# Performance work log

Hardware: AMD Instinct MI355X
Metric: run time of the kernel (lower is better)

The kernel has to match this reference:

```python
import jax, jax.numpy as jnp
import numpy as np

B, D = 16384, 2048          # batch, input_dim
N_TOP, N_CLASS = 8, 16      # top labels, bottom labels per top (uniform, contiguous ids)

def setup_inputs() -> dict:
    key = jax.random.key(0)
    k1, k2, k3, k4, k5 = jax.random.split(key, 5)
    INIT = 0.2  # matches init_weight uniform(-0.2, 0.2)
    return {
        "features": jax.random.normal(k1, (B, D), dtype=jnp.float32),
        "top_W": jax.random.uniform(k2, (N_TOP, D), minval=-INIT, maxval=INIT, dtype=jnp.float32),
        "top_b": jax.random.uniform(k3, (N_TOP,), minval=-INIT, maxval=INIT, dtype=jnp.float32),
        "bottom_W": jax.random.uniform(k4, (N_TOP, D, N_CLASS), minval=-INIT, maxval=INIT, dtype=jnp.float32),
        "bottom_b": jax.random.uniform(k5, (N_TOP, N_CLASS), minval=-INIT, maxval=INIT, dtype=jnp.float32),
    }

def reference(features, top_W, top_b, bottom_W, bottom_b):
    # dropout p=0.0 -> identity
    # top gate: linear + sigmoid, (b, n_top)
    top_scores = jax.nn.sigmoid(features @ top_W.T + top_b)
    # all per-top-label expert linears as one batched GEMM: (b, n_top, n_class)
    bottom_logits = jnp.einsum('bd,tdc->btc', features, bottom_W) + bottom_b
    bottom_scores = jax.nn.softmax(bottom_logits, axis=-1)
    # scatter-combine: bottom ids of top i are contiguous [i*N_CLASS, (i+1)*N_CLASS),
    # so the column scatter is a reshape. (b, n_bottom_labels)
    final_scores = (top_scores[:, :, None] * bottom_scores).reshape(features.shape[0], N_TOP * N_CLASS)
    return final_scores
```

## Files before the change

kernel.cpp:

```cpp
#include <hip/hip_runtime.h>


#define D_DIM 2048
#define NTILE 9
#define NCOLS 144

using f32x4 = float __attribute__((ext_vector_type(4)));
using half8 = _Float16 __attribute__((ext_vector_type(8)));

__global__ void prep_weights(const float* __restrict__ topW,
                             const float* __restrict__ botW,
                             _Float16* __restrict__ S) {
    int idx = blockIdx.x * blockDim.x + threadIdx.x;
    if (idx >= 4 * 16 * NTILE * 64) return;
    int lane = idx & 63;
    int tmp  = idx >> 6;
    int nt   = tmp % NTILE;
    int wks  = tmp / NTILE;
    int n     = nt * 16 + (lane & 15);
    int kbase = wks * 32 + (lane >> 4) * 8;

    _Float16 v[8];
    #pragma unroll
    for (int j = 0; j < 8; j++) {
        int k = kbase + j;
        float x = 0.0f;
        if (n < 8) {
            x = topW[n * D_DIM + k];
        } else if (n < 136) {
            int t = (n - 8) >> 4, c = (n - 8) & 15;
            x = botW[(t * D_DIM + k) * 16 + c];
        }
        v[j] = (_Float16)x;
    }
    *(half8*)(S + (size_t)idx * 8) = *(half8*)v;
}

__global__ __launch_bounds__(256, 4) void hc_fused(
        const float* __restrict__ feat, const _Float16* __restrict__ Bsw,
        const float* __restrict__ top_b, const float* __restrict__ bot_b,
        float* __restrict__ out) {
    __shared__ float red[4][16][148];

    const int tid  = threadIdx.x;
    const int lane = tid & 63, wave = tid >> 6;
    const int quad = lane >> 4, low = lane & 15;
    const size_t row0 = (size_t)blockIdx.x * 16;

    const f32x4* Ap = (const f32x4*)(feat + (row0 + low) * D_DIM + wave * 512 + quad * 8);
    const _Float16* Bw = Bsw + (size_t)wave * (16 * NTILE * 512) + lane * 8;

    f32x4 acc[NTILE];
    #pragma unroll
    for (int i = 0; i < NTILE; i++) acc[i] = (f32x4)0.0f;

    #pragma unroll 4
    for (int ks = 0; ks < 16; ks++) {
        f32x4 a0 = Ap[ks * 8];
        f32x4 a1 = Ap[ks * 8 + 1];
        half8 bf[NTILE];
        #pragma unroll
        for (int nt = 0; nt < NTILE; nt++)
            bf[nt] = *(const half8*)(Bw + (ks * NTILE + nt) * 512);
        half8 af;
        af[0] = (_Float16)a0[0]; af[1] = (_Float16)a0[1];
        af[2] = (_Float16)a0[2]; af[3] = (_Float16)a0[3];
        af[4] = (_Float16)a1[0]; af[5] = (_Float16)a1[1];
        af[6] = (_Float16)a1[2]; af[7] = (_Float16)a1[3];
        #pragma unroll
        for (int nt = 0; nt < NTILE; nt++)
            acc[nt] = __builtin_amdgcn_mfma_f32_16x16x32_f16(af, bf[nt], acc[nt], 0, 0, 0);
    }

    #pragma unroll
    for (int nt = 0; nt < NTILE; nt++) {
        #pragma unroll
        for (int r = 0; r < 4; r++) {
            red[wave][quad * 4 + r][nt * 16 + low] = acc[nt][r];
        }
    }
    __syncthreads();

    const int row = tid >> 4;
    const int top = tid & 15;
    if (top < 8) {
        float zt = top_b[top];
        #pragma unroll
        for (int w = 0; w < 4; w++) zt += red[w][row][top];
        const float sig = 1.0f / (1.0f + __expf(-zt));

        float z[16];
        float zmax = -1e30f;
        #pragma unroll
        for (int c = 0; c < 16; c++) {
            float v = bot_b[top * 16 + c];
            #pragma unroll
            for (int w = 0; w < 4; w++) v += red[w][row][8 + top * 16 + c];
            z[c] = v;
            zmax = fmaxf(zmax, v);
        }
        float s = 0.0f;
        #pragma unroll
        for (int c = 0; c < 16; c++) { z[c] = __expf(z[c] - zmax); s += z[c]; }
        const float scale = sig / s;

        float* o = out + (row0 + row) * 128 + top * 16;
        #pragma unroll
        for (int c = 0; c < 16; c += 4) {
            f32x4 v = { z[c] * scale, z[c+1] * scale, z[c+2] * scale, z[c+3] * scale };
            *(f32x4*)(o + c) = v;
        }
    }
}

extern "C" void kernel_launch(void* const* d_in, const int* in_sizes, int n_in,
                              void* d_out, int out_size, void* d_ws, size_t ws_size,
                              hipStream_t stream) {
    const float* feat  = (const float*)d_in[0];
    const float* topW  = (const float*)d_in[1];
    const float* topB  = (const float*)d_in[2];
    const float* botW  = (const float*)d_in[3];
    const float* botB  = (const float*)d_in[4];
    float* out = (float*)d_out;
    _Float16* Bsw = (_Float16*)d_ws;

    prep_weights<<<(4 * 16 * NTILE * 64 + 255) / 256, 256, 0, stream>>>(topW, botW, Bsw);
    hc_fused<<<16384 / 16, 256, 0, stream>>>(feat, Bsw, topB, botB, out);
}
```

Measured before the change: 214.8 us.

## Process 32 rows per block to reuse weight fragments across two M tiles

Each block now computes two 16-row M tiles, so every loaded fp16 weight fragment feeds two MFMAs instead of one, halving weight traffic per row. The grid shrinks to 512 blocks, launch bounds drop to 2 blocks per SM to make room for the doubled accumulators, and the epilogue now uses all 256 threads (32 rows x 8 tops). This raises register and LDS pressure and lowers occupancy, and the kernel is likely bound by reading features, so the gain may be small.

```diff
diff --git a/kernel.cpp b/kernel.cpp
--- a/kernel.cpp
+++ b/kernel.cpp
@@ -4,6 +4,7 @@
 #define D_DIM 2048
 #define NTILE 9
 #define NCOLS 144
+#define M_ROWS 32
 
 using f32x4 = float __attribute__((ext_vector_type(4)));
 using half8 = _Float16 __attribute__((ext_vector_type(8)));
@@ -36,54 +37,64 @@
     *(half8*)(S + (size_t)idx * 8) = *(half8*)v;
 }
 
-__global__ __launch_bounds__(256, 4) void hc_fused(
+__global__ __launch_bounds__(256, 2) void hc_fused(
         const float* __restrict__ feat, const _Float16* __restrict__ Bsw,
         const float* __restrict__ top_b, const float* __restrict__ bot_b,
         float* __restrict__ out) {
-    __shared__ float red[4][16][148];
+    __shared__ float red[4][M_ROWS][148];
 
     const int tid  = threadIdx.x;
     const int lane = tid & 63, wave = tid >> 6;
     const int quad = lane >> 4, low = lane & 15;
-    const size_t row0 = (size_t)blockIdx.x * 16;
+    const size_t row0 = (size_t)blockIdx.x * M_ROWS;
 
-    const f32x4* Ap = (const f32x4*)(feat + (row0 + low) * D_DIM + wave * 512 + quad * 8);
+    const f32x4* Ap0 = (const f32x4*)(feat + (row0 + low) * D_DIM + wave * 512 + quad * 8);
+    const f32x4* Ap1 = (const f32x4*)(feat + (row0 + 16 + low) * D_DIM + wave * 512 + quad * 8);
     const _Float16* Bw = Bsw + (size_t)wave * (16 * NTILE * 512) + lane * 8;
 
-    f32x4 acc[NTILE];
+    f32x4 acc0[NTILE], acc1[NTILE];
     #pragma unroll
-    for (int i = 0; i < NTILE; i++) acc[i] = (f32x4)0.0f;
+    for (int i = 0; i < NTILE; i++) { acc0[i] = (f32x4)0.0f; acc1[i] = (f32x4)0.0f; }
 
-    #pragma unroll 4
+    #pragma unroll 2
     for (int ks = 0; ks < 16; ks++) {
-        f32x4 a0 = Ap[ks * 8];
-        f32x4 a1 = Ap[ks * 8 + 1];
+        f32x4 a00 = Ap0[ks * 8];
+        f32x4 a01 = Ap0[ks * 8 + 1];
+        f32x4 a10 = Ap1[ks * 8];
+        f32x4 a11 = Ap1[ks * 8 + 1];
         half8 bf[NTILE];
         #pragma unroll
         for (int nt = 0; nt < NTILE; nt++)
             bf[nt] = *(const half8*)(Bw + (ks * NTILE + nt) * 512);
-        half8 af;
-        af[0] = (_Float16)a0[0]; af[1] = (_Float16)a0[1];
-        af[2] = (_Float16)a0[2]; af[3] = (_Float16)a0[3];
-        af[4] = (_Float16)a1[0]; af[5] = (_Float16)a1[1];
-        af[6] = (_Float16)a1[2]; af[7] = (_Float16)a1[3];
+        half8 af0, af1;
+        af0[0] = (_Float16)a00[0]; af0[1] = (_Float16)a00[1];
+        af0[2] = (_Float16)a00[2]; af0[3] = (_Float16)a00[3];
+        af0[4] = (_Float16)a01[0]; af0[5] = (_Float16)a01[1];
+        af0[6] = (_Float16)a01[2]; af0[7] = (_Float16)a01[3];
+        af1[0] = (_Float16)a10[0]; af1[1] = (_Float16)a10[1];
+        af1[2] = (_Float16)a10[2]; af1[3] = (_Float16)a10[3];
+        af1[4] = (_Float16)a11[0]; af1[5] = (_Float16)a11[1];
+        af1[6] = (_Float16)a11[2]; af1[7] = (_Float16)a11[3];
         #pragma unroll
-        for (int nt = 0; nt < NTILE; nt++)
-            acc[nt] = __builtin_amdgcn_mfma_f32_16x16x32_f16(af, bf[nt], acc[nt], 0, 0, 0);
+        for (int nt = 0; nt < NTILE; nt++) {
+            acc0[nt] = __builtin_amdgcn_mfma_f32_16x16x32_f16(af0, bf[nt], acc0[nt], 0, 0, 0);
+            acc1[nt] = __builtin_amdgcn_mfma_f32_16x16x32_f16(af1, bf[nt], acc1[nt], 0, 0, 0);
+        }
     }
 
     #pragma unroll
     for (int nt = 0; nt < NTILE; nt++) {
         #pragma unroll
         for (int r = 0; r < 4; r++) {
-            red[wave][quad * 4 + r][nt * 16 + low] = acc[nt][r];
+            red[wave][quad * 4 + r][nt * 16 + low]      = acc0[nt][r];
+            red[wave][16 + quad * 4 + r][nt * 16 + low] = acc1[nt][r];
         }
     }
     __syncthreads();
 
-    const int row = tid >> 4;
-    const int top = tid & 15;
-    if (top < 8) {
+    const int row = tid >> 3;
+    const int top = tid & 7;
+    {
         float zt = top_b[top];
         #pragma unroll
         for (int w = 0; w < 4; w++) zt += red[w][row][top];
@@ -125,5 +136,5 @@
     _Float16* Bsw = (_Float16*)d_ws;
 
     prep_weights<<<(4 * 16 * NTILE * 64 + 255) / 256, 256, 0, stream>>>(topW, botW, Bsw);
-    hc_fused<<<16384 / 16, 256, 0, stream>>>(feat, Bsw, topB, botB, out);
+    hc_fused<<<16384 / M_ROWS, 256, 0, stream>>>(feat, Bsw, topB, botB, out);
 }
```

Result: faster. 209.5 us (-2.5%).
